# Optimization experiments

Hardware: AMD Instinct MI355X
Metric: run time of the kernel (lower is better)

## Reference

```python
import jax, jax.numpy as jnp
import numpy as np

N, PAIR_DIM, H, D = 256, 128, 4, 32
EPS = 1e-5


def setup_inputs() -> dict:
    key = jax.random.key(0)
    ks = jax.random.split(key, 10)
    s = 1.0 / np.sqrt(PAIR_DIM)
    return {
        "pair_embed": jax.random.normal(ks[0], (N, N, PAIR_DIM), jnp.float32),
        "ln_scale": jnp.ones((PAIR_DIM,), jnp.float32),
        "ln_bias": jnp.zeros((PAIR_DIM,), jnp.float32),
        "Wq": jax.random.normal(ks[1], (PAIR_DIM, H * D), jnp.float32) * s,
        "Wk": jax.random.normal(ks[2], (PAIR_DIM, H * D), jnp.float32) * s,
        "Wv": jax.random.normal(ks[3], (PAIR_DIM, H * D), jnp.float32) * s,
        "Wb": jax.random.normal(ks[4], (PAIR_DIM, H), jnp.float32) * s,
        "Wg": jax.random.normal(ks[5], (PAIR_DIM, H * D), jnp.float32) * s,
        "bg": jnp.zeros((H * D,), jnp.float32),
        "Wo": jax.random.normal(ks[6], (H * D, PAIR_DIM), jnp.float32) * s,
        "bo": jnp.zeros((PAIR_DIM,), jnp.float32),
    }


def _layernorm(x, scale, bias):
    mu = jnp.mean(x, axis=-1, keepdims=True)
    var = jnp.mean(jnp.square(x - mu), axis=-1, keepdims=True)
    return (x - mu) * jax.lax.rsqrt(var + EPS) * scale + bias


def reference(pair_embed, ln_scale, ln_bias, Wq, Wk, Wv, Wb, Wg, bg, Wo, bo):
    n = pair_embed.shape[0]
    z = _layernorm(pair_embed, ln_scale, ln_bias)          # [N,N,C]
    q = (z @ Wq).reshape(n, n, H, D) * (1.0 / np.sqrt(D))  # [N,N,H,D]
    k = (z @ Wk).reshape(n, n, H, D)
    v = (z @ Wv).reshape(n, n, H, D)
    # pair bias: [N,N,H] -> [H,1,N,N], broadcast over row index i
    bias = jnp.transpose(z @ Wb, (2, 0, 1))[:, None, :, :]
    logits = jnp.einsum('ijhd,ikhd->hijk', q, k) + bias    # [H,N,N,N]
    attn = jax.nn.softmax(logits, axis=-1)
    gate = jax.nn.sigmoid(z @ Wg + bg).reshape(n, n, H, D)
    out = jnp.einsum('hijk,ikhd->ijhd', attn, v) * gate    # [N,N,H,D]
    out = out.reshape(n, n, H * D)
    return out @ Wo + bo                                   # [N,N,C]
```

## Files before the change

### kernel.cpp

```cpp
#include <hip/hip_runtime.h>
#include <hip/hip_bf16.h>


typedef _Float16 half8 __attribute__((ext_vector_type(8)));
typedef _Float16 half4 __attribute__((ext_vector_type(4)));
typedef float floatx4 __attribute__((ext_vector_type(4)));

#define NN 256
#define CC 128
#define HH 4
#define DD 32
#define NR (NN*NN)
#define LN_EPS 1e-5f
#define MFMA(a,b,c) __builtin_amdgcn_mfma_f32_16x16x32_f16(a,b,c,0,0,0)
#define ZERO4 ((floatx4)(0.f))

__device__ inline half4 cvt4(floatx4 v) {
    half4 r; r[0]=(_Float16)v[0]; r[1]=(_Float16)v[1];
    r[2]=(_Float16)v[2]; r[3]=(_Float16)v[3]; return r;
}

__global__ __launch_bounds__(256) void prep_weights(
    const float* __restrict__ Wq, const float* __restrict__ Wk,
    const float* __restrict__ Wv, const float* __restrict__ Wg,
    const float* __restrict__ Wo, const float* __restrict__ Wb,
    _Float16* __restrict__ WqT, _Float16* __restrict__ WkT,
    _Float16* __restrict__ WvT, _Float16* __restrict__ WgT,
    _Float16* __restrict__ WoT, _Float16* __restrict__ WbT)
{
    int id = blockIdx.x * 256 + threadIdx.x;
    if (id < 5 * 16384) {
        int m = id / 16384, e = id % 16384;
        int n = e >> 7, c = e & 127;
        const float* src = (m==0)?Wq:(m==1)?Wk:(m==2)?Wv:(m==3)?Wg:Wo;
        _Float16* dst    = (m==0)?WqT:(m==1)?WkT:(m==2)?WvT:(m==3)?WgT:WoT;
        dst[n*128 + c] = (_Float16)src[c*128 + n];
    } else {
        int e = id - 5*16384;
        if (e < 16*128) {
            int n = e >> 7, c = e & 127;
            WbT[n*128 + c] = (n < HH) ? (_Float16)Wb[c*HH + n] : (_Float16)0.f;
        }
    }
}

__global__ __launch_bounds__(256) void bias_ln_kernel(
    const float* __restrict__ pair, const float* __restrict__ ln_scale,
    const float* __restrict__ ln_bias, const _Float16* __restrict__ WbT,
    _Float16* __restrict__ zh, float* __restrict__ biasF)
{
    int wave = threadIdx.x >> 6, lane = threadIdx.x & 63;
    int mtile = blockIdx.x * 4 + wave;
    int lr = lane & 15, lg = lane >> 4;
    size_t row = (size_t)mtile*16 + lr;

    float xv[4][8];
    float s = 0.f, ss = 0.f;
    #pragma unroll
    for (int ks = 0; ks < 4; ++ks) {
        const float* pr = &pair[row*CC + ks*32 + lg*8];
        float4 a = *(const float4*)pr;
        float4 b = *(const float4*)(pr + 4);
        xv[ks][0]=a.x; xv[ks][1]=a.y; xv[ks][2]=a.z; xv[ks][3]=a.w;
        xv[ks][4]=b.x; xv[ks][5]=b.y; xv[ks][6]=b.z; xv[ks][7]=b.w;
        s  += a.x+a.y+a.z+a.w + b.x+b.y+b.z+b.w;
        ss += a.x*a.x+a.y*a.y+a.z*a.z+a.w*a.w + b.x*b.x+b.y*b.y+b.z*b.z+b.w*b.w;
    }
    s  += __shfl_xor(s, 16);  s  += __shfl_xor(s, 32);
    ss += __shfl_xor(ss, 16); ss += __shfl_xor(ss, 32);
    float mu   = s * (1.f/128.f);
    float var  = ss * (1.f/128.f) - mu*mu;
    float rstd = rsqrtf(var + LN_EPS);

    half8 zfrag[4];
    #pragma unroll
    for (int ks = 0; ks < 4; ++ks) {
        const float* sc = &ln_scale[ks*32 + lg*8];
        const float* bi = &ln_bias[ks*32 + lg*8];
        #pragma unroll
        for (int e = 0; e < 8; ++e)
            zfrag[ks][e] = (_Float16)((xv[ks][e] - mu) * rstd * sc[e] + bi[e]);
        *(half8*)&zh[row*CC + ks*32 + lg*8] = zfrag[ks];
    }

    floatx4 acc2 = ZERO4;
    #pragma unroll
    for (int ks = 0; ks < 4; ++ks) {
        half8 w = *(const half8*)&WbT[lr*128 + ks*32 + lg*8];
        acc2 = MFMA(w, zfrag[ks], acc2);
    }
    if (lg == 0) {
        #pragma unroll
        for (int r = 0; r < 4; ++r)
            biasF[(size_t)r*NR + row] = acc2[r];
    }
}

__global__ __launch_bounds__(512, 2) void mega_kernel(
    const _Float16* __restrict__ zh,
    const _Float16* __restrict__ WqT, const _Float16* __restrict__ WkT,
    const _Float16* __restrict__ WvT, const _Float16* __restrict__ WgT,
    const _Float16* __restrict__ WoT,
    const float* __restrict__ bg, const float* __restrict__ biasF,
    const float* __restrict__ bo, float* __restrict__ out)
{
    __shared__ _Float16 Ksm[256*32];
    __shared__ _Float16 Vt[32*264];
    __shared__ _Float16 scr[8*16*96];

    const int tid  = threadIdx.x;
    const int wave = tid >> 6, lane = tid & 63;
    const int lr   = lane & 15, lg = lane >> 4;
    const int wbase = wave * 32;
    const size_t rb = (size_t)blockIdx.x * NN;
    const int sbase = wave*(16*96) + lr*96;

    half8 zf[2][4];
    #pragma unroll
    for (int at = 0; at < 2; ++at)
        #pragma unroll
        for (int ks = 0; ks < 4; ++ks)
            zf[at][ks] = *(const half8*)&zh[(rb + wbase + at*16 + lr)*CC + ks*32 + lg*8];

    half8 ofrag[4][2];

    #pragma unroll
    for (int h = 0; h < HH; ++h) {
        half8 qf[2];
        #pragma unroll
        for (int at = 0; at < 2; ++at) {
            floatx4 qa[2];
            #pragma unroll
            for (int ntl = 0; ntl < 2; ++ntl) {
                floatx4 a = ZERO4;
                #pragma unroll
                for (int ks = 0; ks < 4; ++ks)
                    a = MFMA(*(const half8*)&WqT[((2*h+ntl)*16 + lr)*CC + ks*32 + lg*8],
                             zf[at][ks], a);
                qa[ntl] = a * 0.17677669529663687f;
            }
            int sb = sbase + (at&1)*48;
            *(half4*)&scr[sb + lg*4]      = cvt4(qa[0]);
            *(half4*)&scr[sb + 16 + lg*4] = cvt4(qa[1]);
            qf[at] = *(const half8*)&scr[sb + lg*8];
        }

        half4 gt[2][2];
        #pragma unroll
        for (int at = 0; at < 2; ++at)
            #pragma unroll
            for (int ntl = 0; ntl < 2; ++ntl) {
                floatx4 a = ZERO4;
                #pragma unroll
                for (int ks = 0; ks < 4; ++ks)
                    a = MFMA(*(const half8*)&WgT[((2*h+ntl)*16 + lr)*CC + ks*32 + lg*8],
                             zf[at][ks], a);
                floatx4 b4 = *(const floatx4*)&bg[(2*h+ntl)*16 + lg*4];
                half4 g4;
                #pragma unroll
                for (int r = 0; r < 4; ++r)
                    g4[r] = (_Float16)(1.f/(1.f + __expf(-(a[r] + b4[r]))));
                gt[at][ntl] = g4;
            }

        __syncthreads();

        #pragma unroll
        for (int at = 0; at < 2; ++at) {
            int kk = wbase + at*16 + lr;
            int swz = (kk >> 1) & 3;
            #pragma unroll
            for (int ntl = 0; ntl < 2; ++ntl) {
                floatx4 a = ZERO4;
                #pragma unroll
                for (int ks = 0; ks < 4; ++ks)
                    a = MFMA(*(const half8*)&WkT[((2*h+ntl)*16 + lr)*CC + ks*32 + lg*8],
                             zf[at][ks], a);
                int chunk = ntl*2 + (lg>>1);
                *(half4*)&Ksm[(kk*4 + (chunk ^ swz))*8 + (lg&1)*4] = cvt4(a);
            }
        }
        #pragma unroll
        for (int at = 0; at < 2; ++at) {
            int k0 = wbase + at*16 + lg*4;
            #pragma unroll
            for (int ntl = 0; ntl < 2; ++ntl) {
                floatx4 a = ZERO4;
                #pragma unroll
                for (int ks = 0; ks < 4; ++ks)
                    a = MFMA(zf[at][ks],
                             *(const half8*)&WvT[((2*h+ntl)*16 + lr)*CC + ks*32 + lg*8], a);
                int d = ntl*16 + lr;
                *(half4*)&Vt[d*264 + k0] = cvt4(a);
            }
        }

        __syncthreads();

        #pragma unroll
        for (int at = 0; at < 2; ++at) {
            int j = wbase + at*16 + lr;
            floatx4 sacc[16];
            #pragma unroll
            for (int nt = 0; nt < 16; ++nt) {
                int kk = nt*16 + lr;
                half8 kf = *(const half8*)&Ksm[(kk*4 + (lg ^ ((kk>>1)&3)))*8];
                floatx4 a = MFMA(kf, qf[at], ZERO4);
                a += *(const floatx4*)&biasF[((size_t)h*NN + j)*NN + nt*16 + lg*4];
                sacc[nt] = a;
            }
            float m = -1e30f;
            #pragma unroll
            for (int nt = 0; nt < 16; ++nt)
                #pragma unroll
                for (int r = 0; r < 4; ++r) m = fmaxf(m, sacc[nt][r]);
            m = fmaxf(m, __shfl_xor(m, 16));
            m = fmaxf(m, __shfl_xor(m, 32));
            float l = 0.f;
            #pragma unroll
            for (int nt = 0; nt < 16; ++nt)
                #pragma unroll
                for (int r = 0; r < 4; ++r) {
                    float p = __expf(sacc[nt][r] - m);
                    sacc[nt][r] = p; l += p;
                }
            l += __shfl_xor(l, 16);
            l += __shfl_xor(l, 32);
            float linv = 1.f / l;

            floatx4 oacc0 = ZERO4;
            floatx4 oacc1 = ZERO4;
            #pragma unroll
            for (int g = 0; g < 8; ++g) {
                int sb = sbase + (g&1)*48;
                *(half4*)&scr[sb + lg*4]      = cvt4(sacc[2*g]);
                *(half4*)&scr[sb + 16 + lg*4] = cvt4(sacc[2*g+1]);
                half8 pf = *(const half8*)&scr[sb + lg*8];
                half8 vf0 = *(const half8*)&Vt[(lr)*264      + g*32 + lg*8];
                half8 vf1 = *(const half8*)&Vt[(16+lr)*264   + g*32 + lg*8];
                oacc0 = MFMA(vf0, pf, oacc0);
                oacc1 = MFMA(vf1, pf, oacc1);
            }
            half4 pk0, pk1;
            #pragma unroll
            for (int r = 0; r < 4; ++r) {
                pk0[r] = (_Float16)(oacc0[r] * linv * (float)gt[at][0][r]);
                pk1[r] = (_Float16)(oacc1[r] * linv * (float)gt[at][1][r]);
            }
            *(half4*)&scr[sbase + lg*4]      = pk0;
            *(half4*)&scr[sbase + 16 + lg*4] = pk1;
            ofrag[h][at] = *(const half8*)&scr[sbase + lg*8];
        }
    }

    #pragma unroll
    for (int at = 0; at < 2; ++at) {
        size_t orow = rb + wbase + at*16 + lr;
        #pragma unroll
        for (int nt = 0; nt < 8; ++nt) {
            floatx4 a = ZERO4;
            #pragma unroll
            for (int ks = 0; ks < 4; ++ks)
                a = MFMA(*(const half8*)&WoT[(nt*16 + lr)*CC + ks*32 + lg*8],
                         ofrag[ks][at], a);
            int col = nt*16 + lg*4;
            a += *(const floatx4*)&bo[col];
            *(floatx4*)&out[orow*CC + col] = a;
        }
    }
}

extern "C" void kernel_launch(void* const* d_in, const int* in_sizes, int n_in,
                              void* d_out, int out_size, void* d_ws, size_t ws_size,
                              hipStream_t stream)
{
    const float* pair     = (const float*)d_in[0];
    const float* ln_scale = (const float*)d_in[1];
    const float* ln_bias  = (const float*)d_in[2];
    const float* Wq       = (const float*)d_in[3];
    const float* Wk       = (const float*)d_in[4];
    const float* Wv       = (const float*)d_in[5];
    const float* Wb       = (const float*)d_in[6];
    const float* Wg       = (const float*)d_in[7];
    const float* bg       = (const float*)d_in[8];
    const float* Wo       = (const float*)d_in[9];
    const float* bo       = (const float*)d_in[10];
    float* out = (float*)d_out;

    char* ws = (char*)d_ws;
    _Float16* zh  = (_Float16*)ws; ws += (size_t)NR * CC * sizeof(_Float16);
    float* biasF  = (float*)ws;    ws += (size_t)HH * NR * sizeof(float);
    _Float16* WqT = (_Float16*)ws; ws += 128*128*sizeof(_Float16);
    _Float16* WkT = (_Float16*)ws; ws += 128*128*sizeof(_Float16);
    _Float16* WvT = (_Float16*)ws; ws += 128*128*sizeof(_Float16);
    _Float16* WgT = (_Float16*)ws; ws += 128*128*sizeof(_Float16);
    _Float16* WoT = (_Float16*)ws; ws += 128*128*sizeof(_Float16);
    _Float16* WbT = (_Float16*)ws; ws += 16*128*sizeof(_Float16);

    prep_weights<<<(5*16384 + 16*128 + 255)/256, 256, 0, stream>>>(
        Wq, Wk, Wv, Wg, Wo, Wb, WqT, WkT, WvT, WgT, WoT, WbT);

    bias_ln_kernel<<<NR/16/4, 256, 0, stream>>>(
        pair, ln_scale, ln_bias, WbT, zh, biasF);

    mega_kernel<<<NN, 512, 0, stream>>>(
        zh, WqT, WkT, WvT, WgT, WoT, bg, biasF, bo, out);
}
```

Measured before the change: 117.5 us.

## Split each attention row across two blocks to raise occupancy

The grid doubles so that each block handles half of the query rows j for one i. Every block still computes the full K and V for its row, reloading z from global for the key tiles. Launch bounds rise to four blocks per CU to cut register use, and the XOR-swizzled K layout is replaced by a padded stride. The trade is more parallelism and occupancy against doubled K/V projection work and possible register spills.

```diff
diff --git a/kernel.cpp b/kernel.cpp
--- a/kernel.cpp
+++ b/kernel.cpp
@@ -14,6 +14,8 @@
 #define LN_EPS 1e-5f
 #define MFMA(a,b,c) __builtin_amdgcn_mfma_f32_16x16x32_f16(a,b,c,0,0,0)
 #define ZERO4 ((floatx4)(0.f))
+#define KSTR 34
+#define SSTR 98
 
 __device__ inline half4 cvt4(floatx4 v) {
     half4 r; r[0]=(_Float16)v[0]; r[1]=(_Float16)v[1];
@@ -96,7 +98,7 @@
     }
 }
 
-__global__ __launch_bounds__(512, 2) void mega_kernel(
+__global__ __launch_bounds__(512, 4) void mega_kernel(
     const _Float16* __restrict__ zh,
     const _Float16* __restrict__ WqT, const _Float16* __restrict__ WkT,
     const _Float16* __restrict__ WvT, const _Float16* __restrict__ WgT,
@@ -104,169 +106,144 @@
     const float* __restrict__ bg, const float* __restrict__ biasF,
     const float* __restrict__ bo, float* __restrict__ out)
 {
-    __shared__ _Float16 Ksm[256*32];
+    __shared__ _Float16 Ksm[256*KSTR];
     __shared__ _Float16 Vt[32*264];
-    __shared__ _Float16 scr[8*16*96];
+    __shared__ _Float16 scr[8*16*SSTR];
 
     const int tid  = threadIdx.x;
     const int wave = tid >> 6, lane = tid & 63;
     const int lr   = lane & 15, lg = lane >> 4;
-    const int wbase = wave * 32;
-    const size_t rb = (size_t)blockIdx.x * NN;
-    const int sbase = wave*(16*96) + lr*96;
-
-    half8 zf[2][4];
-    #pragma unroll
-    for (int at = 0; at < 2; ++at)
+    const int ib   = blockIdx.x >> 1;
+    const int jh   = blockIdx.x & 1;
+    const int jbase = jh*128 + wave*16;
+    const int kbase = wave*32;
+    const size_t rb = (size_t)ib * NN;
+    const int sbase = wave*(16*SSTR) + lr*SSTR;
+
+    half8 zfj[4];
+    #pragma unroll
+    for (int ks = 0; ks < 4; ++ks)
+        zfj[ks] = *(const half8*)&zh[(rb + jbase + lr)*CC + ks*32 + lg*8];
+
+    half8 ofrag[4];
+
+    #pragma unroll
+    for (int h = 0; h < HH; ++h) {
+        floatx4 qa0 = ZERO4, qa1 = ZERO4;
+        #pragma unroll
+        for (int ks = 0; ks < 4; ++ks) {
+            qa0 = MFMA(*(const half8*)&WqT[((2*h+0)*16 + lr)*CC + ks*32 + lg*8], zfj[ks], qa0);
+            qa1 = MFMA(*(const half8*)&WqT[((2*h+1)*16 + lr)*CC + ks*32 + lg*8], zfj[ks], qa1);
+        }
+        qa0 *= 0.17677669529663687f;
+        qa1 *= 0.17677669529663687f;
+        *(half4*)&scr[sbase + lg*4]      = cvt4(qa0);
+        *(half4*)&scr[sbase + 16 + lg*4] = cvt4(qa1);
+        half8 qf = *(const half8*)&scr[sbase + lg*8];
+
+        floatx4 ga0 = ZERO4, ga1 = ZERO4;
+        #pragma unroll
+        for (int ks = 0; ks < 4; ++ks) {
+            ga0 = MFMA(*(const half8*)&WgT[((2*h+0)*16 + lr)*CC + ks*32 + lg*8], zfj[ks], ga0);
+            ga1 = MFMA(*(const half8*)&WgT[((2*h+1)*16 + lr)*CC + ks*32 + lg*8], zfj[ks], ga1);
+        }
+        floatx4 bg0 = *(const floatx4*)&bg[(2*h+0)*16 + lg*4];
+        floatx4 bg1 = *(const floatx4*)&bg[(2*h+1)*16 + lg*4];
+        half4 gt0, gt1;
+        #pragma unroll
+        for (int r = 0; r < 4; ++r) {
+            gt0[r] = (_Float16)(1.f/(1.f + __expf(-(ga0[r] + bg0[r]))));
+            gt1[r] = (_Float16)(1.f/(1.f + __expf(-(ga1[r] + bg1[r]))));
+        }
+
+        __syncthreads();
+
+        #pragma unroll
+        for (int at = 0; at < 2; ++at) {
+            half8 zk[4];
+            #pragma unroll
+            for (int ks = 0; ks < 4; ++ks)
+                zk[ks] = *(const half8*)&zh[(rb + kbase + at*16 + lr)*CC + ks*32 + lg*8];
+            floatx4 ak0 = ZERO4, ak1 = ZERO4, av0 = ZERO4, av1 = ZERO4;
+            #pragma unroll
+            for (int ks = 0; ks < 4; ++ks) {
+                ak0 = MFMA(*(const half8*)&WkT[((2*h+0)*16 + lr)*CC + ks*32 + lg*8], zk[ks], ak0);
+                ak1 = MFMA(*(const half8*)&WkT[((2*h+1)*16 + lr)*CC + ks*32 + lg*8], zk[ks], ak1);
+                av0 = MFMA(zk[ks], *(const half8*)&WvT[((2*h+0)*16 + lr)*CC + ks*32 + lg*8], av0);
+                av1 = MFMA(zk[ks], *(const half8*)&WvT[((2*h+1)*16 + lr)*CC + ks*32 + lg*8], av1);
+            }
+            int kk = kbase + at*16 + lr;
+            *(half4*)&Ksm[kk*KSTR + lg*4]      = cvt4(ak0);
+            *(half4*)&Ksm[kk*KSTR + 16 + lg*4] = cvt4(ak1);
+            int k0 = kbase + at*16 + lg*4;
+            *(half4*)&Vt[lr*264 + k0]        = cvt4(av0);
+            *(half4*)&Vt[(16 + lr)*264 + k0] = cvt4(av1);
+        }
+
+        __syncthreads();
+
+        int j = jbase + lr;
+        floatx4 sacc[16];
+        #pragma unroll
+        for (int nt = 0; nt < 16; ++nt) {
+            half8 kf = *(const half8*)&Ksm[(nt*16 + lr)*KSTR + lg*8];
+            floatx4 a = MFMA(kf, qf, ZERO4);
+            a += *(const floatx4*)&biasF[((size_t)h*NN + j)*NN + nt*16 + lg*4];
+            sacc[nt] = a;
+        }
+        float m = -1e30f;
+        #pragma unroll
+        for (int nt = 0; nt < 16; ++nt)
+            #pragma unroll
+            for (int r = 0; r < 4; ++r) m = fmaxf(m, sacc[nt][r]);
+        m = fmaxf(m, __shfl_xor(m, 16));
+        m = fmaxf(m, __shfl_xor(m, 32));
+        float l = 0.f;
+        #pragma unroll
+        for (int nt = 0; nt < 16; ++nt)
+            #pragma unroll
+            for (int r = 0; r < 4; ++r) {
+                float p = __expf(sacc[nt][r] - m);
+                sacc[nt][r] = p; l += p;
+            }
+        l += __shfl_xor(l, 16);
+        l += __shfl_xor(l, 32);
+        float linv = 1.f / l;
+
+        floatx4 oacc0 = ZERO4, oacc1 = ZERO4;
+        #pragma unroll
+        for (int g = 0; g < 8; ++g) {
+            int sb = sbase + (g&1)*48;
+            *(half4*)&scr[sb + lg*4]      = cvt4(sacc[2*g]);
+            *(half4*)&scr[sb + 16 + lg*4] = cvt4(sacc[2*g+1]);
+            half8 pf  = *(const half8*)&scr[sb + lg*8];
+            half8 vf0 = *(const half8*)&Vt[lr*264        + g*32 + lg*8];
+            half8 vf1 = *(const half8*)&Vt[(16+lr)*264   + g*32 + lg*8];
+            oacc0 = MFMA(vf0, pf, oacc0);
+            oacc1 = MFMA(vf1, pf, oacc1);
+        }
+        half4 pk0, pk1;
+        #pragma unroll
+        for (int r = 0; r < 4; ++r) {
+            pk0[r] = (_Float16)(oacc0[r] * linv * (float)gt0[r]);
+            pk1[r] = (_Float16)(oacc1[r] * linv * (float)gt1[r]);
+        }
+        *(half4*)&scr[sbase + lg*4]      = pk0;
+        *(half4*)&scr[sbase + 16 + lg*4] = pk1;
+        ofrag[h] = *(const half8*)&scr[sbase + lg*8];
+    }
+
+    size_t orow = rb + jbase + lr;
+    #pragma unroll
+    for (int nt = 0; nt < 8; ++nt) {
+        floatx4 a = ZERO4;
         #pragma unroll
         for (int ks = 0; ks < 4; ++ks)
-            zf[at][ks] = *(const half8*)&zh[(rb + wbase + at*16 + lr)*CC + ks*32 + lg*8];
-
-    half8 ofrag[4][2];
-
-    #pragma unroll
-    for (int h = 0; h < HH; ++h) {
-        half8 qf[2];
-        #pragma unroll
-        for (int at = 0; at < 2; ++at) {
-            floatx4 qa[2];
-            #pragma unroll
-            for (int ntl = 0; ntl < 2; ++ntl) {
-                floatx4 a = ZERO4;
-                #pragma unroll
-                for (int ks = 0; ks < 4; ++ks)
-                    a = MFMA(*(const half8*)&WqT[((2*h+ntl)*16 + lr)*CC + ks*32 + lg*8],
-                             zf[at][ks], a);
-                qa[ntl] = a * 0.17677669529663687f;
-            }
-            int sb = sbase + (at&1)*48;
-            *(half4*)&scr[sb + lg*4]      = cvt4(qa[0]);
-            *(half4*)&scr[sb + 16 + lg*4] = cvt4(qa[1]);
-            qf[at] = *(const half8*)&scr[sb + lg*8];
-        }
-
-        half4 gt[2][2];
-        #pragma unroll
-        for (int at = 0; at < 2; ++at)
-            #pragma unroll
-            for (int ntl = 0; ntl < 2; ++ntl) {
-                floatx4 a = ZERO4;
-                #pragma unroll
-                for (int ks = 0; ks < 4; ++ks)
-                    a = MFMA(*(const half8*)&WgT[((2*h+ntl)*16 + lr)*CC + ks*32 + lg*8],
-                             zf[at][ks], a);
-                floatx4 b4 = *(const floatx4*)&bg[(2*h+ntl)*16 + lg*4];
-                half4 g4;
-                #pragma unroll
-                for (int r = 0; r < 4; ++r)
-                    g4[r] = (_Float16)(1.f/(1.f + __expf(-(a[r] + b4[r]))));
-                gt[at][ntl] = g4;
-            }
-
-        __syncthreads();
-
-        #pragma unroll
-        for (int at = 0; at < 2; ++at) {
-            int kk = wbase + at*16 + lr;
-            int swz = (kk >> 1) & 3;
-            #pragma unroll
-            for (int ntl = 0; ntl < 2; ++ntl) {
-                floatx4 a = ZERO4;
-                #pragma unroll
-                for (int ks = 0; ks < 4; ++ks)
-                    a = MFMA(*(const half8*)&WkT[((2*h+ntl)*16 + lr)*CC + ks*32 + lg*8],
-                             zf[at][ks], a);
-                int chunk = ntl*2 + (lg>>1);
-                *(half4*)&Ksm[(kk*4 + (chunk ^ swz))*8 + (lg&1)*4] = cvt4(a);
-            }
-        }
-        #pragma unroll
-        for (int at = 0; at < 2; ++at) {
-            int k0 = wbase + at*16 + lg*4;
-            #pragma unroll
-            for (int ntl = 0; ntl < 2; ++ntl) {
-                floatx4 a = ZERO4;
-                #pragma unroll
-                for (int ks = 0; ks < 4; ++ks)
-                    a = MFMA(zf[at][ks],
-                             *(const half8*)&WvT[((2*h+ntl)*16 + lr)*CC + ks*32 + lg*8], a);
-                int d = ntl*16 + lr;
-                *(half4*)&Vt[d*264 + k0] = cvt4(a);
-            }
-        }
-
-        __syncthreads();
-
-        #pragma unroll
-        for (int at = 0; at < 2; ++at) {
-            int j = wbase + at*16 + lr;
-            floatx4 sacc[16];
-            #pragma unroll
-            for (int nt = 0; nt < 16; ++nt) {
-                int kk = nt*16 + lr;
-                half8 kf = *(const half8*)&Ksm[(kk*4 + (lg ^ ((kk>>1)&3)))*8];
-                floatx4 a = MFMA(kf, qf[at], ZERO4);
-                a += *(const floatx4*)&biasF[((size_t)h*NN + j)*NN + nt*16 + lg*4];
-                sacc[nt] = a;
-            }
-            float m = -1e30f;
-            #pragma unroll
-            for (int nt = 0; nt < 16; ++nt)
-                #pragma unroll
-                for (int r = 0; r < 4; ++r) m = fmaxf(m, sacc[nt][r]);
-            m = fmaxf(m, __shfl_xor(m, 16));
-            m = fmaxf(m, __shfl_xor(m, 32));
-            float l = 0.f;
-            #pragma unroll
-            for (int nt = 0; nt < 16; ++nt)
-                #pragma unroll
-                for (int r = 0; r < 4; ++r) {
-                    float p = __expf(sacc[nt][r] - m);
-                    sacc[nt][r] = p; l += p;
-                }
-            l += __shfl_xor(l, 16);
-            l += __shfl_xor(l, 32);
-            float linv = 1.f / l;
-
-            floatx4 oacc0 = ZERO4;
-            floatx4 oacc1 = ZERO4;
-            #pragma unroll
-            for (int g = 0; g < 8; ++g) {
-                int sb = sbase + (g&1)*48;
-                *(half4*)&scr[sb + lg*4]      = cvt4(sacc[2*g]);
-                *(half4*)&scr[sb + 16 + lg*4] = cvt4(sacc[2*g+1]);
-                half8 pf = *(const half8*)&scr[sb + lg*8];
-                half8 vf0 = *(const half8*)&Vt[(lr)*264      + g*32 + lg*8];
-                half8 vf1 = *(const half8*)&Vt[(16+lr)*264   + g*32 + lg*8];
-                oacc0 = MFMA(vf0, pf, oacc0);
-                oacc1 = MFMA(vf1, pf, oacc1);
-            }
-            half4 pk0, pk1;
-            #pragma unroll
-            for (int r = 0; r < 4; ++r) {
-                pk0[r] = (_Float16)(oacc0[r] * linv * (float)gt[at][0][r]);
-                pk1[r] = (_Float16)(oacc1[r] * linv * (float)gt[at][1][r]);
-            }
-            *(half4*)&scr[sbase + lg*4]      = pk0;
-            *(half4*)&scr[sbase + 16 + lg*4] = pk1;
-            ofrag[h][at] = *(const half8*)&scr[sbase + lg*8];
-        }
-    }
-
-    #pragma unroll
-    for (int at = 0; at < 2; ++at) {
-        size_t orow = rb + wbase + at*16 + lr;
-        #pragma unroll
-        for (int nt = 0; nt < 8; ++nt) {
-            floatx4 a = ZERO4;
-            #pragma unroll
-            for (int ks = 0; ks < 4; ++ks)
-                a = MFMA(*(const half8*)&WoT[(nt*16 + lr)*CC + ks*32 + lg*8],
-                         ofrag[ks][at], a);
-            int col = nt*16 + lg*4;
-            a += *(const floatx4*)&bo[col];
-            *(floatx4*)&out[orow*CC + col] = a;
-        }
+            a = MFMA(*(const half8*)&WoT[(nt*16 + lr)*CC + ks*32 + lg*8],
+                     ofrag[ks], a);
+        int col = nt*16 + lg*4;
+        a += *(const floatx4*)&bo[col];
+        *(floatx4*)&out[orow*CC + col] = a;
     }
 }
 
@@ -303,6 +280,6 @@
     bias_ln_kernel<<<NR/16/4, 256, 0, stream>>>(
         pair, ln_scale, ln_bias, WbT, zh, biasF);
 
-    mega_kernel<<<NN, 512, 0, stream>>>(
+    mega_kernel<<<2*NN, 512, 0, stream>>>(
         zh, WqT, WkT, WvT, WgT, WoT, bg, biasF, bo, out);
 }
```

After: 174.9 us. 1.49x slower.
